# Performance work log

Measured on AMD Instinct MI355X. Metric: run time of the kernel, lower is better.

## Reference

```python
import jax, jax.numpy as jnp
import numpy as np

B_SZ, L, H, P = 8, 8192, 1024, 64  # batch, seq, d_inner, ssm_size
CONJ_SYM = True
DT_MIN, DT_MAX, DT_FLOOR = 1e-3, 1e-1, 1e-4


def setup_inputs() -> dict:
    key = jax.random.key(0)
    ks = jax.random.split(key, 8)
    u = jax.random.normal(ks[0], (B_SZ, L, H), dtype=jnp.float32)
    h_real = jnp.zeros((B_SZ, P), dtype=jnp.float32)
    h_imag = jnp.zeros((B_SZ, P), dtype=jnp.float32)
    # HiPPO-like stable init: Re(Lambda) = -0.5, Im(Lambda) = pi*k
    A_real = -0.5 * jnp.ones((P,), dtype=jnp.float32)
    A_imag = jnp.pi * jnp.arange(P, dtype=jnp.float32)
    local_P = 2 * P if CONJ_SYM else P
    b_scale = np.sqrt(1.0 / local_P).astype(np.float32)
    c_scale = np.sqrt(1.0 / H).astype(np.float32)
    B_real = jax.random.normal(ks[1], (P, H), dtype=jnp.float32) * b_scale
    B_imag = jax.random.normal(ks[2], (P, H), dtype=jnp.float32) * b_scale
    C_real = jax.random.normal(ks[3], (H, P), dtype=jnp.float32) * c_scale
    C_imag = jax.random.normal(ks[4], (H, P), dtype=jnp.float32) * c_scale
    D = jax.random.normal(ks[5], (H,), dtype=jnp.float32)
    # torch init: dt = exp(U(log dt_min, log dt_max)).clamp(dt_floor); inv_dt = dt + log(-expm1(-dt))
    log_dt = jax.random.uniform(ks[6], (P,), dtype=jnp.float32) \
        * (np.log(DT_MAX) - np.log(DT_MIN)) + np.log(DT_MIN)
    dt0 = jnp.clip(jnp.exp(log_dt), DT_FLOOR, None)
    inv_dt = dt0 + jnp.log(-jnp.expm1(-dt0))
    return {"u": u, "h_real": h_real, "h_imag": h_imag,
            "A_real": A_real, "A_imag": A_imag,
            "B_real": B_real, "B_imag": B_imag,
            "C_real": C_real, "C_imag": C_imag,
            "D": D, "inv_dt": inv_dt}


def reference(u, h_real, h_imag, A_real, A_imag, B_real, B_imag,
              C_real, C_imag, D, inv_dt):
    A = A_real + 1j * A_imag            # (P,)
    Bm = B_real + 1j * B_imag           # (P, H)
    Cm = C_real + 1j * C_imag           # (H, P)
    dt = jax.nn.softplus(inv_dt)        # step_rescale = 1.0
    # bilinear discretization
    den = 1.0 - (dt / 2.0) * A
    dA = (1.0 + (dt / 2.0) * A) / den   # (P,)
    dB = (dt / den)[:, None] * Bm       # (P, H)
    # input projection: Bu[b,l,p] = sum_h dB[p,h] * u[b,l,h]
    Bu = jnp.einsum('blh,ph->blp', u, dB)              # complex64 (B, L, P)
    h0 = h_real + 1j * h_imag                          # (B, P)
    Bu = Bu.at[:, 0].add(dA * h0)                      # fold initial state in
    a = jnp.broadcast_to(dA, Bu.shape)
    def combine(e1, e2):
        a1, b1 = e1
        a2, b2 = e2
        return a2 * a1, a2 * b1 + b2
    _, hs = jax.lax.associative_scan(combine, (a, Bu), axis=1)  # (B, L, P)
    yc = jnp.einsum('blp,hp->blh', hs, Cm)
    scale = 2.0 if CONJ_SYM else 1.0
    y = scale * yc.real + D * u
    h_last = hs[:, -1]
    return y, h_last.real, h_last.imag
```

## Files before the change

### kernel.cpp

```cpp
#include <hip/hip_runtime.h>

typedef unsigned short ushort_t;
typedef short s8v __attribute__((ext_vector_type(8)));
typedef unsigned short ushort8 __attribute__((ext_vector_type(8)));
typedef float floatx4 __attribute__((ext_vector_type(4)));

#define MFMA16(a, b, c) __builtin_amdgcn_mfma_f32_16x16x32_bf16((a), (b), (c), 0, 0, 0)

static constexpr int B_SZ = 8;
static constexpr int L = 8192;
static constexpr int H = 1024;
static constexpr int M_TOT = B_SZ * L;
static constexpr int S_CH = 128;
static constexpr int NC = L / S_CH;

__device__ inline ushort_t f2bf(float f) {
    union { float f; unsigned u; } v; v.f = f;
    unsigned r = v.u + 0x7fffu + ((v.u >> 16) & 1u);
    return (ushort_t)(r >> 16);
}

__device__ inline unsigned cvtpk(float lo, float hi) {
    unsigned r;
    asm("v_cvt_pk_bf16_f32 %0, %1, %2" : "=v"(r) : "v"(lo), "v"(hi));
    return r;
}

typedef union { s8v v; unsigned u[4]; } u32x4;

__device__ inline void gload_lds16(const void* g, void* l) {
    __builtin_amdgcn_global_load_lds(
        (const __attribute__((address_space(1))) void*)g,
        (__attribute__((address_space(3))) void*)l, 16, 0, 0);
}

__global__ void params_kernel(const float* __restrict__ A_real,
                              const float* __restrict__ A_imag,
                              const float* __restrict__ inv_dt,
                              float* __restrict__ params,
                              float* __restrict__ dApow) {
    int p = threadIdx.x;
    float x = inv_dt[p];
    float dt = (x > 20.f) ? x : log1pf(expf(x));
    float ar = A_real[p], ai = A_imag[p];
    float dr = 1.f - 0.5f * dt * ar;
    float di = -0.5f * dt * ai;
    float inv = 1.f / fmaf(dr, dr, di * di);
    float nr = 1.f + 0.5f * dt * ar, ni = 0.5f * dt * ai;
    float dAr = (nr * dr + ni * di) * inv;
    float dAi = (ni * dr - nr * di) * inv;
    params[p]       = dAr;
    params[64 + p]  = dAi;
    params[128 + p] = dt * dr * inv;
    params[192 + p] = -dt * di * inv;
    float pr = 1.f, pi = 0.f;
    dApow[2 * p] = 1.f; dApow[2 * p + 1] = 0.f;
    for (int k = 1; k <= S_CH; k++) {
        float npr = pr * dAr - pi * dAi;
        float npi = pr * dAi + pi * dAr;
        pr = npr; pi = npi;
        dApow[k * 128 + 2 * p]     = pr;
        dApow[k * 128 + 2 * p + 1] = pi;
    }
}

__global__ void build_w(const float* __restrict__ Br, const float* __restrict__ Bi,
                        const float* __restrict__ Cr, const float* __restrict__ Ci,
                        const float* __restrict__ params,
                        ushort_t* __restrict__ W1T, ushort_t* __restrict__ CeffT) {
    int t = blockIdx.x * 256 + threadIdx.x;
    if (t < 128 * 1024) {
        int n = t >> 10, k = t & 1023;
        int p = n >> 1;
        float sr = params[128 + p], si = params[192 + p];
        float br = Br[p * 1024 + k], bi = Bi[p * 1024 + k];
        float v = (n & 1) ? (sr * bi + si * br) : (sr * br - si * bi);
        W1T[t] = f2bf(v);
    } else {
        int t2 = t - 128 * 1024;
        int ct_ti = t2 >> 9, g = t2 & 511;
        int ct = ct_ti >> 2, ti = ct_ti & 3;
        int n = g >> 2;
        int h = ct * 128 + n;
        int qq = (g & 3) ^ ((n >> 1) & 3);
        int kb = ti * 32 + qq * 8;
        ushort8 o;
        #pragma unroll
        for (int e = 0; e < 8; e++) {
            int k = kb + e;
            int p = k >> 1;
            float v = (k & 1) ? -2.f * Ci[h * 64 + p] : 2.f * Cr[h * 64 + p];
            o[e] = f2bf(v);
        }
        *(ushort8*)&CeffT[t2 * 8] = o;
    }
}

__global__ __launch_bounds__(256) void gemm1s(const float* __restrict__ u,
                                              const ushort_t* __restrict__ W1T,
                                              const float* __restrict__ params,
                                              const float* __restrict__ dApow,
                                              float* __restrict__ hloc,
                                              float* __restrict__ endbuf) {
    __shared__ float bus[128 * 128];
    ushort_t* As = (ushort_t*)bus;
    ushort_t* Bs = As + 128 * 40;
    int tid = threadIdx.x;
    int wave = tid >> 6, lane = tid & 63;
    int q = lane >> 4, mn = lane & 15;
    size_t row0 = (size_t)blockIdx.x * 128;
    int r = tid >> 1, half = tid & 1;

    floatx4 acc[2][8] = {};

    for (int kk = 0; kk < 1024; kk += 32) {
        __syncthreads();
        {
            const float4* up = (const float4*)(u + (row0 + r) * 1024 + kk + half * 16);
            float4 f0 = up[0], f1 = up[1], f2 = up[2], f3 = up[3];
            u32x4 t0, t1;
            t0.u[0] = cvtpk(f0.x, f0.y); t0.u[1] = cvtpk(f0.z, f0.w);
            t0.u[2] = cvtpk(f1.x, f1.y); t0.u[3] = cvtpk(f1.z, f1.w);
            t1.u[0] = cvtpk(f2.x, f2.y); t1.u[1] = cvtpk(f2.z, f2.w);
            t1.u[2] = cvtpk(f3.x, f3.y); t1.u[3] = cvtpk(f3.z, f3.w);
            s8v* dst = (s8v*)&As[r * 40 + half * 16];
            dst[0] = t0.v; dst[1] = t1.v;
            const ushort8* wp = (const ushort8*)(W1T + r * 1024 + kk + half * 16);
            ushort8* db = (ushort8*)&Bs[r * 40 + half * 16];
            db[0] = wp[0]; db[1] = wp[1];
        }
        __syncthreads();
        s8v a0 = *(const s8v*)&As[(wave * 32 + mn) * 40 + q * 8];
        s8v a1 = *(const s8v*)&As[(wave * 32 + 16 + mn) * 40 + q * 8];
        #pragma unroll
        for (int j = 0; j < 8; j++) {
            s8v bf = *(const s8v*)&Bs[(j * 16 + mn) * 40 + q * 8];
            acc[0][j] = MFMA16(a0, bf, acc[0][j]);
            acc[1][j] = MFMA16(a1, bf, acc[1][j]);
        }
    }
    __syncthreads();
    #pragma unroll
    for (int i = 0; i < 2; i++)
        #pragma unroll
        for (int j = 0; j < 8; j++)
            #pragma unroll
            for (int reg = 0; reg < 4; reg++) {
                int row = wave * 32 + i * 16 + q * 4 + reg;
                bus[row * 128 + j * 16 + mn] = acc[i][j][reg];
            }
    __syncthreads();

    float dAr = params[lane], dAi = params[64 + lane];
    float hr = 0.f, hi = 0.f;
    int base = wave * 32 * 128 + 2 * lane;
    #pragma unroll 8
    for (int t = 0; t < 32; t++) {
        float2 v = *(float2*)&bus[base + t * 128];
        float nhr = fmaf(dAr, hr, fmaf(-dAi, hi, v.x));
        float nhi = fmaf(dAr, hi, fmaf(dAi, hr, v.y));
        hr = nhr; hi = nhi;
        *(float2*)&bus[base + t * 128] = make_float2(hr, hi);
    }
    __syncthreads();

    float a32r = dApow[32 * 128 + 2 * lane], a32i = dApow[32 * 128 + 2 * lane + 1];
    float cr = 0.f, ci = 0.f;
    for (int w2 = 0; w2 < wave; w2++) {
        float2 e = *(float2*)&bus[(w2 * 32 + 31) * 128 + 2 * lane];
        float tr = fmaf(a32r, cr, fmaf(-a32i, ci, e.x));
        float ti = fmaf(a32r, ci, fmaf(a32i, cr, e.y));
        cr = tr; ci = ti;
    }

    float* gbase = hloc + (row0 + wave * 32) * 128 + 2 * lane;
    float lr = 0.f, li = 0.f;
    float pr = dAr, pi = dAi;
    #pragma unroll 8
    for (int t = 0; t < 32; t++) {
        float2 v = *(float2*)&bus[base + t * 128];
        float orr = v.x + pr * cr - pi * ci;
        float oi  = v.y + pr * ci + pi * cr;
        *(float2*)(gbase + (size_t)t * 128) = make_float2(orr, oi);
        lr = orr; li = oi;
        float npr = pr * dAr - pi * dAi;
        float npi = pr * dAi + pi * dAr;
        pr = npr; pi = npi;
    }
    if (wave == 3) {
        float* e = endbuf + (size_t)blockIdx.x * 128 + 2 * lane;
        e[0] = lr; e[1] = li;
    }
}

__global__ void scan_carry(const float* __restrict__ endbuf,
                           const float* __restrict__ dApow,
                           const float* __restrict__ h0r,
                           const float* __restrict__ h0i,
                           float* __restrict__ carry) {
    int t = blockIdx.x * 64 + threadIdx.x;
    int b = t >> 6, p = t & 63;
    float aSr = dApow[S_CH * 128 + 2 * p], aSi = dApow[S_CH * 128 + 2 * p + 1];
    float cr = h0r[b * 64 + p], ci = h0i[b * 64 + p];
    #pragma unroll
    for (int half = 0; half < 2; half++) {
        float2 e[32];
        #pragma unroll
        for (int c = 0; c < 32; c++)
            e[c] = *(const float2*)(endbuf + ((size_t)b * NC + half * 32 + c) * 128 + 2 * p);
        #pragma unroll
        for (int c = 0; c < 32; c++) {
            int cc = half * 32 + c;
            *(float2*)(carry + ((size_t)b * NC + cc) * 128 + 2 * p) = make_float2(cr, ci);
            float nr = fmaf(aSr, cr, fmaf(-aSi, ci, e[c].x));
            float ni = fmaf(aSr, ci, fmaf(aSi, cr, e[c].y));
            cr = nr; ci = ni;
        }
    }
}

__global__ __launch_bounds__(256, 4) void gemm2t(const float* __restrict__ hloc,
                                                 const ushort_t* __restrict__ CeffT,
                                                 const float* __restrict__ u,
                                                 const float* __restrict__ D,
                                                 const float* __restrict__ dApow,
                                                 const float* __restrict__ carry,
                                                 float* __restrict__ y,
                                                 float* __restrict__ out_hlast) {
    __shared__ __align__(16) char smem[64 * 132 * 4];
    ushort_t* Blds = (ushort_t*)smem;
    float* ldsF = (float*)smem;
    int tid = threadIdx.x;
    int w = tid >> 6, lane = tid & 63;
    int q = lane >> 4, mn = lane & 15;
    int swz = q ^ ((mn >> 1) & 3);
    size_t row0 = (size_t)blockIdx.x * 64;
    int b = (int)(row0 >> 13);
    int l0 = (int)(row0 & (L - 1));
    int c = l0 >> 7;

    int seq = w * 16 + mn;
    int l = l0 + seq;
    int kp = (l & (S_CH - 1)) + 1;
    const float* hrow = hloc + (row0 + seq) * 128;
    const float* prow = dApow + (size_t)kp * 128;
    const float* crow = carry + ((size_t)b * NC + c) * 128;
    bool last = (l == L - 1);

    u32x4 Bf[4];
    #pragma unroll
    for (int kt = 0; kt < 4; kt++) {
        int kb = kt * 32 + q * 8;
        float4 h0 = *(const float4*)(hrow + kb);
        float4 h1 = *(const float4*)(hrow + kb + 4);
        float4 p0 = *(const float4*)(prow + kb);
        float4 p1 = *(const float4*)(prow + kb + 4);
        float4 c0 = *(const float4*)(crow + kb);
        float4 c1 = *(const float4*)(crow + kb + 4);
        float f0 = h0.x + p0.x * c0.x - p0.y * c0.y;
        float f1 = h0.y + p0.x * c0.y + p0.y * c0.x;
        float f2 = h0.z + p0.z * c0.z - p0.w * c0.w;
        float f3 = h0.w + p0.z * c0.w + p0.w * c0.z;
        float f4 = h1.x + p1.x * c1.x - p1.y * c1.y;
        float f5 = h1.y + p1.x * c1.y + p1.y * c1.x;
        float f6 = h1.z + p1.z * c1.z - p1.w * c1.w;
        float f7 = h1.w + p1.z * c1.w + p1.w * c1.z;
        Bf[kt].u[0] = cvtpk(f0, f1); Bf[kt].u[1] = cvtpk(f2, f3);
        Bf[kt].u[2] = cvtpk(f4, f5); Bf[kt].u[3] = cvtpk(f6, f7);
        if (last) {
            int pb = kb >> 1;
            out_hlast[b * 64 + pb]     = f0; out_hlast[512 + b * 64 + pb]     = f1;
            out_hlast[b * 64 + pb + 1] = f2; out_hlast[512 + b * 64 + pb + 1] = f3;
            out_hlast[b * 64 + pb + 2] = f4; out_hlast[512 + b * 64 + pb + 2] = f5;
            out_hlast[b * 64 + pb + 3] = f6; out_hlast[512 + b * 64 + pb + 3] = f7;
        }
    }

    int erow_b = w * 16 + (lane >> 5);
    int es4 = lane & 31;

    for (int ct = 0; ct < 8; ct++) {
        const float* ub = u + ct * 128 + es4 * 4;
        float4 uv0 = *(const float4*)(ub + (row0 + erow_b + 0) * 1024);
        float4 uv1 = *(const float4*)(ub + (row0 + erow_b + 2) * 1024);
        float4 uv2 = *(const float4*)(ub + (row0 + erow_b + 4) * 1024);
        float4 uv3 = *(const float4*)(ub + (row0 + erow_b + 6) * 1024);
        float4 dvv = *(const float4*)(D + ct * 128 + es4 * 4);

        if (ct) __syncthreads();
        {
            const ushort_t* gsrc = CeffT + (size_t)ct * 16384 + w * 512 + lane * 8;
            ushort_t* ldst = Blds + w * 512;
            #pragma unroll
            for (int it = 0; it < 8; it++)
                gload_lds16(gsrc + it * 2048, ldst + it * 2048);
        }
        __syncthreads();
        floatx4 acc[8] = {};
        #pragma unroll
        for (int kt = 0; kt < 4; kt++) {
            int bofs = kt * 4096 + swz * 8;
            #pragma unroll
            for (int j = 0; j < 8; j++) {
                s8v af = *(const s8v*)&Blds[bofs + (j * 16 + mn) * 32];
                acc[j] = MFMA16(af, Bf[kt].v, acc[j]);
            }
        }
        __syncthreads();
        #pragma unroll
        for (int j = 0; j < 8; j++)
            *(floatx4*)&ldsF[(size_t)seq * 132 + j * 16 + q * 4] = acc[j];
        __syncthreads();
        #pragma unroll
        for (int i = 0; i < 8; i++) {
            int row = erow_b + i * 2;
            float4 fv = *(const float4*)&ldsF[(size_t)row * 132 + es4 * 4];
            float4 uvv = (i == 0) ? uv0 : (i == 1) ? uv1 : (i == 2) ? uv2 :
                         (i == 3) ? uv3 :
                         *(const float4*)(ub + (row0 + row) * 1024);
            float4 o;
            o.x = fv.x + dvv.x * uvv.x;
            o.y = fv.y + dvv.y * uvv.y;
            o.z = fv.z + dvv.z * uvv.z;
            o.w = fv.w + dvv.w * uvv.w;
            *(float4*)(y + (row0 + row) * 1024 + ct * 128 + es4 * 4) = o;
        }
    }
}

extern "C" void kernel_launch(void* const* d_in, const int* in_sizes, int n_in,
                              void* d_out, int out_size, void* d_ws, size_t ws_size,
                              hipStream_t stream) {
    const float* u      = (const float*)d_in[0];
    const float* h_r    = (const float*)d_in[1];
    const float* h_i    = (const float*)d_in[2];
    const float* A_real = (const float*)d_in[3];
    const float* A_imag = (const float*)d_in[4];
    const float* B_real = (const float*)d_in[5];
    const float* B_imag = (const float*)d_in[6];
    const float* C_real = (const float*)d_in[7];
    const float* C_imag = (const float*)d_in[8];
    const float* D      = (const float*)d_in[9];
    const float* inv_dt = (const float*)d_in[10];
    float* out = (float*)d_out;

    float* wsf       = (float*)d_ws;
    float* P_params  = wsf;
    float* P_dApow   = wsf + 1024;
    float* P_carry   = wsf + 1024 + 16640;
    float* P_end     = P_carry + 65536;
    ushort_t* P_W1T  = (ushort_t*)(P_end + 65536);
    ushort_t* P_Ceff = P_W1T + 128 * 1024;
    float* P_Bu      = (float*)(P_Ceff + 1024 * 128);

    params_kernel<<<1, 64, 0, stream>>>(A_real, A_imag, inv_dt, P_params, P_dApow);
    build_w<<<576, 256, 0, stream>>>(B_real, B_imag, C_real, C_imag, P_params, P_W1T, P_Ceff);
    gemm1s<<<M_TOT / 128, 256, 0, stream>>>(u, P_W1T, P_params, P_dApow, P_Bu, P_end);
    scan_carry<<<8, 64, 0, stream>>>(P_end, P_dApow, h_r, h_i, P_carry);
    gemm2t<<<M_TOT / 64, 256, 0, stream>>>(P_Bu, P_Ceff, u, D, P_dApow, P_carry,
                                           out, out + (size_t)M_TOT * H);
}
```

Measured before the change: 596.0 us.

## Double-buffer gemm1s K-loop with direct global-to-LDS loads and swizzled fp32 tiles

```diff
diff --git a/kernel.cpp b/kernel.cpp
--- a/kernel.cpp
+++ b/kernel.cpp
@@ -102,44 +102,70 @@
                                               const float* __restrict__ dApow,
                                               float* __restrict__ hloc,
                                               float* __restrict__ endbuf) {
-    __shared__ float bus[128 * 128];
-    ushort_t* As = (ushort_t*)bus;
-    ushort_t* Bs = As + 128 * 40;
+    __shared__ __align__(16) char smem[65536];
+    float* bus = (float*)smem;
     int tid = threadIdx.x;
     int wave = tid >> 6, lane = tid & 63;
     int q = lane >> 4, mn = lane & 15;
     size_t row0 = (size_t)blockIdx.x * 128;
-    int r = tid >> 1, half = tid & 1;
+
+    int srA = lane >> 3;
+    int sinA = (((lane & 7) ^ srA) << 4);
+    int srB = lane >> 2;
+    int sinB = (lane & 3) << 4;
 
     floatx4 acc[2][8] = {};
 
-    for (int kk = 0; kk < 1024; kk += 32) {
+    int r0 = wave * 32 + mn;
+    int maskA = (r0 & 7) << 4;
+    int ya0 = r0 * 128 + q * 32;
+    int ya1 = (r0 + 16) * 128 + q * 32;
+
+    #define STAGE1(buf, kk)                                                     \
+        do {                                                                    \
+            _Pragma("unroll")                                                   \
+            for (int i_ = 0; i_ < 4; i_++) {                                    \
+                int c_ = i_ * 4 + wave;                                         \
+                const char* g_ = (const char*)u +                               \
+                    (row0 + c_ * 8 + srA) * 4096 + (kk) * 4 + sinA;             \
+                gload_lds16(g_, smem + (buf) * 16384 + c_ * 1024);              \
+            }                                                                   \
+            _Pragma("unroll")                                                   \
+            for (int i_ = 0; i_ < 2; i_++) {                                    \
+                int c_ = i_ * 4 + wave;                                         \
+                const char* g_ = (const char*)W1T +                             \
+                    (size_t)(c_ * 16 + srB) * 2048 + (kk) * 2 + sinB;           \
+                gload_lds16(g_, smem + 32768 + (buf) * 8192 + c_ * 1024);       \
+            }                                                                   \
+        } while (0)
+
+    STAGE1(0, 0);
+    __syncthreads();
+    int cur = 0;
+    for (int t = 0; t < 32; t++) {
+        if (t < 31) STAGE1(cur ^ 1, (t + 1) * 32);
+        const char* abase = smem + cur * 16384;
+        floatx4 v00 = *(const floatx4*)(abase + (ya0 ^ maskA));
+        floatx4 v01 = *(const floatx4*)(abase + ((ya0 + 16) ^ maskA));
+        floatx4 v10 = *(const floatx4*)(abase + (ya1 ^ maskA));
+        floatx4 v11 = *(const floatx4*)(abase + ((ya1 + 16) ^ maskA));
+        u32x4 a0, a1;
+        a0.u[0] = cvtpk(v00[0], v00[1]); a0.u[1] = cvtpk(v00[2], v00[3]);
+        a0.u[2] = cvtpk(v01[0], v01[1]); a0.u[3] = cvtpk(v01[2], v01[3]);
+        a1.u[0] = cvtpk(v10[0], v10[1]); a1.u[1] = cvtpk(v10[2], v10[3]);
+        a1.u[2] = cvtpk(v11[0], v11[1]); a1.u[3] = cvtpk(v11[2], v11[3]);
+        const ushort_t* bb = (const ushort_t*)(smem + 32768 + cur * 8192);
+        #pragma unroll
+        for (int j = 0; j < 8; j++) {
+            s8v bf = *(const s8v*)(bb + (j * 16 + mn) * 32 + q * 8);
+            acc[0][j] = MFMA16(a0.v, bf, acc[0][j]);
+            acc[1][j] = MFMA16(a1.v, bf, acc[1][j]);
+        }
         __syncthreads();
-        {
-            const float4* up = (const float4*)(u + (row0 + r) * 1024 + kk + half * 16);
-            float4 f0 = up[0], f1 = up[1], f2 = up[2], f3 = up[3];
-            u32x4 t0, t1;
-            t0.u[0] = cvtpk(f0.x, f0.y); t0.u[1] = cvtpk(f0.z, f0.w);
-            t0.u[2] = cvtpk(f1.x, f1.y); t0.u[3] = cvtpk(f1.z, f1.w);
-            t1.u[0] = cvtpk(f2.x, f2.y); t1.u[1] = cvtpk(f2.z, f2.w);
-            t1.u[2] = cvtpk(f3.x, f3.y); t1.u[3] = cvtpk(f3.z, f3.w);
-            s8v* dst = (s8v*)&As[r * 40 + half * 16];
-            dst[0] = t0.v; dst[1] = t1.v;
-            const ushort8* wp = (const ushort8*)(W1T + r * 1024 + kk + half * 16);
-            ushort8* db = (ushort8*)&Bs[r * 40 + half * 16];
-            db[0] = wp[0]; db[1] = wp[1];
-        }
-        __syncthreads();
-        s8v a0 = *(const s8v*)&As[(wave * 32 + mn) * 40 + q * 8];
-        s8v a1 = *(const s8v*)&As[(wave * 32 + 16 + mn) * 40 + q * 8];
-        #pragma unroll
-        for (int j = 0; j < 8; j++) {
-            s8v bf = *(const s8v*)&Bs[(j * 16 + mn) * 40 + q * 8];
-            acc[0][j] = MFMA16(a0, bf, acc[0][j]);
-            acc[1][j] = MFMA16(a1, bf, acc[1][j]);
-        }
-    }
-    __syncthreads();
+        cur ^= 1;
+    }
+    #undef STAGE1
+
     #pragma unroll
     for (int i = 0; i < 2; i++)
         #pragma unroll
```

New measurement: 595.1 us. About the same (-0.2%).
